# Optimization experiments

Hardware: AMD Instinct MI355X
Metric: run time of the kernel (lower is better)

The kernel has to match this reference:

```python
import jax, jax.numpy as jnp
import numpy as np

CAPACITY_FACTOR = 0.67
AUX_LOSS_COEF = 0.001


def setup_inputs() -> dict:
    key = jax.random.key(0)
    k1, k2 = jax.random.split(key)
    B, S, D = 4, 4096, 2048
    x = jax.random.normal(k1, (B, S, D), dtype=jnp.float32)
    # all-True mask -> static number of active tokens (jit-friendly, same math)
    current_mask = jnp.ones((B, S), dtype=bool)
    w_router = jax.random.normal(k2, (1, D), dtype=jnp.float32) / np.sqrt(D)
    return {"x": x, "current_mask": current_mask, "w_router": w_router}


def reference(x, current_mask, w_router):
    B, S, D = x.shape
    N = B * S
    flat = x.reshape(N, D)
    # router: Linear(d_model, 1, bias=False) then sigmoid -> per-token score
    scores = jax.nn.sigmoid(flat @ w_router[0])  # [N]
    # exclude inactive tokens from selection (mask all-True here, so no-op)
    masked_scores = jnp.where(current_mask.reshape(N), scores, -jnp.inf)
    num_active = N  # static: mask is all-True by construction
    num_to_keep = max(1, int(num_active * CAPACITY_FACTOR))
    top_scores, top_idx = jax.lax.top_k(masked_scores, num_to_keep)
    # scatter selected flat positions into a fresh boolean mask
    new_mask = jnp.zeros(N, dtype=bool).at[top_idx].set(True).reshape(B, S)
    aux_loss = -jnp.mean(top_scores) * AUX_LOSS_COEF
    return new_mask, aux_loss
```

## Files before the change

kernel.cpp:

```cpp
#include <hip/hip_runtime.h>
#include <hip/hip_bf16.h>


#define D_MODEL 2048
#define NSEL_THREADS 1024
#define CHUNK 16

__global__ __launch_bounds__(256) void score_kernel(const float* __restrict__ x,
                                                    const float* __restrict__ w,
                                                    float* __restrict__ scores,
                                                    int n_tok) {
    const int wave = threadIdx.x >> 6;
    const int lane = threadIdx.x & 63;
    const int tok  = blockIdx.x * 4 + wave;
    if (tok >= n_tok) return;

    const float4* xr = (const float4*)(x + (size_t)tok * D_MODEL);
    const float4* wr = (const float4*)w;

    double acc = 0.0;
#pragma unroll
    for (int i = 0; i < D_MODEL / 256; ++i) {
        float4 xv = xr[i * 64 + lane];
        float4 wv = wr[i * 64 + lane];
        acc += (double)xv.x * (double)wv.x + (double)xv.y * (double)wv.y
             + (double)xv.z * (double)wv.z + (double)xv.w * (double)wv.w;
    }
    for (int off = 32; off > 0; off >>= 1)
        acc += __shfl_down(acc, off, 64);

    if (lane == 0) {
        float logit = (float)acc;
        scores[tok] = 1.0f / (1.0f + expf(-logit));
    }
}

__global__ __launch_bounds__(NSEL_THREADS) void select_kernel(const float* __restrict__ scores,
                                                              float* __restrict__ out,
                                                              int n, int k) {
    __shared__ unsigned int whist[16 * 257];
    __shared__ int wsum[16];
    __shared__ unsigned int sel_prefix_sh;
    __shared__ int sel_remaining_sh;
    __shared__ int warp_part[16];
    __shared__ double sum_sh[16];

    const int tid = threadIdx.x;
    const int wv  = tid >> 6;
    const int ln  = tid & 63;
    const int beg = tid * CHUNK;

    unsigned int key[CHUNK];
    {
        const uint4* sv = (const uint4*)(scores + beg);
#pragma unroll
        for (int q = 0; q < CHUNK / 4; ++q) {
            uint4 v = sv[q];
            key[q * 4 + 0] = v.x; key[q * 4 + 1] = v.y;
            key[q * 4 + 2] = v.z; key[q * 4 + 3] = v.w;
        }
    }

    unsigned int prefix = 0;
    unsigned int pmask  = 0;
    int remaining = k;

#pragma unroll
    for (int pass = 0; pass < 4; ++pass) {
        const int shift = 24 - pass * 8;
        for (int i = tid; i < 16 * 257; i += NSEL_THREADS) whist[i] = 0;
        __syncthreads();

        if (pass == 0) {
#pragma unroll
            for (int j = 0; j < CHUNK; ++j) {
                unsigned int dig = key[j] >> 24;
                unsigned long long pending = ~0ull;
                while (pending) {
                    int lead = __ffsll((unsigned long long)pending) - 1;
                    unsigned int d0 = __shfl((int)dig, lead, 64);
                    unsigned long long match = __ballot(dig == d0) & pending;
                    if (ln == lead)
                        atomicAdd(&whist[wv * 257 + d0], (unsigned int)__popcll(match));
                    pending &= ~match;
                }
            }
        } else {
#pragma unroll
            for (int j = 0; j < CHUNK; ++j)
                if ((key[j] & pmask) == prefix)
                    atomicAdd(&whist[wv * 257 + ((key[j] >> shift) & 255u)], 1u);
        }
        __syncthreads();

        int c = 0;
        if (tid < 256) {
#pragma unroll
            for (int w = 0; w < 16; ++w) c += (int)whist[w * 257 + tid];
        }
        int sc = c;
        for (int off = 1; off < 64; off <<= 1) {
            int v = __shfl_down(sc, off, 64);
            if (ln + off < 64) sc += v;
        }
        if (tid < 256 && ln == 0) wsum[wv] = sc;
        __syncthreads();
        if (tid < 256) {
            int hi = 0;
            for (int w = wv + 1; w < 4; ++w) hi += wsum[w];
            const int S_excl = hi + (sc - c);
            if (S_excl < remaining && remaining <= S_excl + c) {
                sel_prefix_sh    = prefix | ((unsigned int)tid << shift);
                sel_remaining_sh = remaining - S_excl;
            }
        }
        __syncthreads();
        prefix    = sel_prefix_sh;
        remaining = sel_remaining_sh;
        pmask    |= (0xFFu << shift);
        __syncthreads();
    }
    const unsigned int tkey = prefix;
    const int ties_needed   = remaining;

    double lsum = 0.0;
#pragma unroll
    for (int j = 0; j < CHUNK; ++j)
        if (key[j] > tkey) lsum += (double)__uint_as_float(key[j]);
    for (int off = 32; off > 0; off >>= 1)
        lsum += __shfl_down(lsum, off, 64);
    if (ln == 0) sum_sh[wv] = lsum;

    int lties = 0;
#pragma unroll
    for (int j = 0; j < CHUNK; ++j)
        if (key[j] == tkey) ++lties;

    int sc2 = lties;
    for (int off = 1; off < 64; off <<= 1) {
        int v = __shfl_up(sc2, off, 64);
        if (ln >= off) sc2 += v;
    }
    if (ln == 63) warp_part[wv] = sc2;
    __syncthreads();
    if (wv == 0 && ln < 16) {
        int v = warp_part[ln];
        for (int off = 1; off < 16; off <<= 1) {
            int u = __shfl_up(v, off, 64);
            if (ln >= off) v += u;
        }
        warp_part[ln] = v;
    }
    __syncthreads();
    const int wave_off = (wv == 0) ? 0 : warp_part[wv - 1];
    const int excl = wave_off + sc2 - lties;

    float mv[CHUNK];
    int taken = 0;
#pragma unroll
    for (int j = 0; j < CHUNK; ++j) {
        if (key[j] > tkey) {
            mv[j] = 1.0f;
        } else if (key[j] == tkey) {
            mv[j] = (excl + taken < ties_needed) ? 1.0f : 0.0f;
            ++taken;
        } else {
            mv[j] = 0.0f;
        }
    }
    {
        float4* ov = (float4*)(out + beg);
#pragma unroll
        for (int q = 0; q < CHUNK / 4; ++q)
            ov[q] = make_float4(mv[q * 4 + 0], mv[q * 4 + 1],
                                mv[q * 4 + 2], mv[q * 4 + 3]);
    }

    if (tid == 0) {
        double s = 0.0;
        for (int i = 0; i < 16; ++i) s += sum_sh[i];
        s += (double)ties_needed * (double)__uint_as_float(tkey);
        out[n] = (float)(-(s / (double)k) * 0.001);
    }
}

extern "C" void kernel_launch(void* const* d_in, const int* in_sizes, int n_in,
                              void* d_out, int out_size, void* d_ws, size_t ws_size,
                              hipStream_t stream) {
    const float* x = (const float*)d_in[0];
    const float* w = (const float*)d_in[2];

    const int d = in_sizes[2];
    const int n = in_sizes[0] / d;

    float* scores = (float*)d_ws;
    float* out    = (float*)d_out;

    int k = (int)((double)n * 0.67);
    if (k < 1) k = 1;

    score_kernel<<<(n + 3) / 4, 256, 0, stream>>>(x, w, scores, n);
    select_kernel<<<1, NSEL_THREADS, 0, stream>>>(scores, out, n, k);
}
```

Baseline: 206.2 us.

## Use three 10-bit radix passes with a single shared histogram

The single-block top-k radix select now does three passes over 10-bit digits instead of four 8-bit passes, and uses one 1024-bin shared histogram (one bin per thread) in place of per-wave 257-bin histograms. The wave-level ballot aggregation in the first pass is removed, along with one barrier per pass. This cuts the number of passes, barriers and histogram reduction loops, at the cost of more shared-atomic contention on one histogram. The first pass reads only bits 20-29, which is correct because sigmoid outputs lie in (0,1) and so have bits 30-31 clear.

```diff
diff --git a/kernel.cpp b/kernel.cpp
--- a/kernel.cpp
+++ b/kernel.cpp
@@ -5,6 +5,7 @@
 #define D_MODEL 2048
 #define NSEL_THREADS 1024
 #define CHUNK 16
+#define NBINS 1024
 
 __global__ __launch_bounds__(256) void score_kernel(const float* __restrict__ x,
                                                     const float* __restrict__ w,
@@ -38,7 +39,7 @@
 __global__ __launch_bounds__(NSEL_THREADS) void select_kernel(const float* __restrict__ scores,
                                                               float* __restrict__ out,
                                                               int n, int k) {
-    __shared__ unsigned int whist[16 * 257];
+    __shared__ unsigned int hist[NBINS];
     __shared__ int wsum[16];
     __shared__ unsigned int sel_prefix_sh;
     __shared__ int sel_remaining_sh;
@@ -66,48 +67,34 @@
     int remaining = k;
 
 #pragma unroll
-    for (int pass = 0; pass < 4; ++pass) {
-        const int shift = 24 - pass * 8;
-        for (int i = tid; i < 16 * 257; i += NSEL_THREADS) whist[i] = 0;
+    for (int pass = 0; pass < 3; ++pass) {
+        const int shift = 20 - pass * 10;
+        hist[tid] = 0;
         __syncthreads();
 
         if (pass == 0) {
 #pragma unroll
-            for (int j = 0; j < CHUNK; ++j) {
-                unsigned int dig = key[j] >> 24;
-                unsigned long long pending = ~0ull;
-                while (pending) {
-                    int lead = __ffsll((unsigned long long)pending) - 1;
-                    unsigned int d0 = __shfl((int)dig, lead, 64);
-                    unsigned long long match = __ballot(dig == d0) & pending;
-                    if (ln == lead)
-                        atomicAdd(&whist[wv * 257 + d0], (unsigned int)__popcll(match));
-                    pending &= ~match;
-                }
-            }
+            for (int j = 0; j < CHUNK; ++j)
+                atomicAdd(&hist[(key[j] >> 20) & (NBINS - 1u)], 1u);
         } else {
 #pragma unroll
             for (int j = 0; j < CHUNK; ++j)
                 if ((key[j] & pmask) == prefix)
-                    atomicAdd(&whist[wv * 257 + ((key[j] >> shift) & 255u)], 1u);
+                    atomicAdd(&hist[(key[j] >> shift) & (NBINS - 1u)], 1u);
         }
         __syncthreads();
 
-        int c = 0;
-        if (tid < 256) {
-#pragma unroll
-            for (int w = 0; w < 16; ++w) c += (int)whist[w * 257 + tid];
-        }
+        const int c = (int)hist[tid];
         int sc = c;
         for (int off = 1; off < 64; off <<= 1) {
             int v = __shfl_down(sc, off, 64);
             if (ln + off < 64) sc += v;
         }
-        if (tid < 256 && ln == 0) wsum[wv] = sc;
+        if (ln == 0) wsum[wv] = sc;
         __syncthreads();
-        if (tid < 256) {
+        {
             int hi = 0;
-            for (int w = wv + 1; w < 4; ++w) hi += wsum[w];
+            for (int w = wv + 1; w < 16; ++w) hi += wsum[w];
             const int S_excl = hi + (sc - c);
             if (S_excl < remaining && remaining <= S_excl + c) {
                 sel_prefix_sh    = prefix | ((unsigned int)tid << shift);
@@ -117,8 +104,7 @@
         __syncthreads();
         prefix    = sel_prefix_sh;
         remaining = sel_remaining_sh;
-        pmask    |= (0xFFu << shift);
-        __syncthreads();
+        pmask    |= ((unsigned int)(NBINS - 1u) << shift);
     }
     const unsigned int tkey = prefix;
     const int ties_needed   = remaining;
```

After: 202.5 us. Within noise of the previous version (-1.8%).
